# Performance work log

Measured on AMD Instinct MI355X. Metric: run time of the kernel, lower is better.

The kernel has to match this reference:

```python
import jax, jax.numpy as jnp
import numpy as np

N = 40000      # nodes
E = 640000     # edges
G = 64         # graphs in batch
F_IN = 128
H = 128


def setup_inputs() -> dict:
    key = jax.random.key(0)
    ks = jax.random.split(key, 10)
    x = jax.random.normal(ks[0], (N, F_IN), dtype=jnp.float32)
    edge_index = jax.random.randint(ks[1], (2, E), 0, N, dtype=jnp.int64)
    batch = jnp.sort(jax.random.randint(ks[2], (N,), 0, G, dtype=jnp.int64))
    s = 0.05
    W1 = jax.random.normal(ks[3], (F_IN, H), dtype=jnp.float32) * s
    W2 = jax.random.normal(ks[4], (H, H), dtype=jnp.float32) * s
    W3 = jax.random.normal(ks[5], (H, H), dtype=jnp.float32) * s
    Wl = jax.random.normal(ks[6], (H, 1), dtype=jnp.float32) * s
    b1 = jnp.zeros((H,), jnp.float32)
    b2 = jnp.zeros((H,), jnp.float32)
    b3 = jnp.zeros((H,), jnp.float32)
    bl = jnp.zeros((1,), jnp.float32)
    return {"x": x, "edge_index": edge_index, "batch": batch, "dropout_rate": 0,
            "W1": W1, "b1": b1, "W2": W2, "b2": b2, "W3": W3, "b3": b3,
            "Wl": Wl, "bl": bl}


def _gcn_norm(edge_index, n):
    # PyG GCNConv default: add self-loops, symmetric deg^{-1/2} normalization.
    loop = jnp.arange(n, dtype=edge_index.dtype)
    row = jnp.concatenate([edge_index[0], loop])  # source
    col = jnp.concatenate([edge_index[1], loop])  # target
    ones = jnp.ones(row.shape[0], jnp.float32)
    deg = jax.ops.segment_sum(ones, col, num_segments=n)
    dis = jnp.where(deg > 0, jax.lax.rsqrt(deg), 0.0)
    norm = dis[row] * dis[col]  # [E+N]
    return row, col, norm


def _gcn_conv(x, row, col, norm, W, b, n):
    h = x @ W + b                       # dense transform [N,H]
    msg = h[row] * norm[:, None]        # gather + scale  [E+N,H]
    return jax.ops.segment_sum(msg, col, num_segments=n)


def reference(x, edge_index, batch, dropout_rate, W1, b1, W2, b2, W3, b3, Wl, bl):
    n = x.shape[0]
    row, col, norm = _gcn_norm(edge_index, n)
    # eval mode: dropout(p=dropout_rate, training=False) is identity
    h = jax.nn.relu(_gcn_conv(x, row, col, norm, W1, b1, n))
    h = jax.nn.relu(_gcn_conv(h, row, col, norm, W2, b2, n))
    h = jax.nn.relu(_gcn_conv(h, row, col, norm, W3, b3, n))
    # global mean pool over graphs
    sums = jax.ops.segment_sum(h, batch, num_segments=G)           # [G,H]
    cnt = jax.ops.segment_sum(jnp.ones(n, jnp.float32), batch, num_segments=G)
    pooled = sums / jnp.maximum(cnt, 1.0)[:, None]
    return pooled @ Wl + bl             # [G,1]
```

## Files before the change

### kernel.cpp

```cpp
#include <hip/hip_runtime.h>

constexpr int N = 40000;
constexpr int E = 640000;
constexpr int G = 64;
constexpr int H = 128;

constexpr int NB      = (N + 255) / 256;
constexpr int EB      = (E + 255) / 256;
constexpr int GEMM1_B = N / 64;
constexpr int FUSED_B = N / 32;
constexpr int CSR_MAX = E + 8 * N;

typedef float    floatx2 __attribute__((ext_vector_type(2)));
typedef float    f32x4   __attribute__((ext_vector_type(4)));
typedef _Float16 f16x8   __attribute__((ext_vector_type(8)));

__device__ __forceinline__ unsigned pack_fp8x4(float a, float b, float c, float d) {
    unsigned v = 0;
    v = __builtin_amdgcn_cvt_pk_fp8_f32(a, b, v, false);
    v = __builtin_amdgcn_cvt_pk_fp8_f32(c, d, v, true);
    return v;
}

__device__ __forceinline__ void fma8(float4& acc, unsigned r, float w) {
    floatx2 lo = __builtin_amdgcn_cvt_pk_f32_fp8(r, false);
    floatx2 hi = __builtin_amdgcn_cvt_pk_f32_fp8(r, true);
    acc.x = fmaf(lo.x, w, acc.x);
    acc.y = fmaf(lo.y, w, acc.y);
    acc.z = fmaf(hi.x, w, acc.z);
    acc.w = fmaf(hi.y, w, acc.w);
}

__device__ __forceinline__ float entry_w(int e) {
    floatx2 hi = __builtin_amdgcn_cvt_pk_f32_fp8((unsigned)e, true);
    return hi.y;
}
__device__ __forceinline__ int entry_src(int e) { return e & 0xFFFFFF; }

__device__ __forceinline__ f16x8 cvt8(float4 a, float4 b) {
    f16x8 r;
    r[0] = (_Float16)a.x; r[1] = (_Float16)a.y; r[2] = (_Float16)a.z; r[3] = (_Float16)a.w;
    r[4] = (_Float16)b.x; r[5] = (_Float16)b.y; r[6] = (_Float16)b.z; r[7] = (_Float16)b.w;
    return r;
}

__device__ __forceinline__ float4 aggregate_node(const unsigned* __restrict__ h8,
                                                 const int4* __restrict__ csr4,
                                                 const int* __restrict__ row_ptr,
                                                 const float* __restrict__ dis,
                                                 int i, int c) {
    float d = dis[i];
    float sl = d * d;
    float4 acc = make_float4(0.f, 0.f, 0.f, 0.f);
    fma8(acc, h8[(size_t)i * 32 + c], sl);
    int p  = row_ptr[i] >> 2;
    int p1 = row_ptr[i + 1] >> 2;
    for (; p < p1; p += 2) {
        int4 ea = csr4[p], eb = csr4[p + 1];
        unsigned r0 = h8[(size_t)entry_src(ea.x) * 32 + c];
        unsigned r1 = h8[(size_t)entry_src(ea.y) * 32 + c];
        unsigned r2 = h8[(size_t)entry_src(ea.z) * 32 + c];
        unsigned r3 = h8[(size_t)entry_src(ea.w) * 32 + c];
        unsigned r4 = h8[(size_t)entry_src(eb.x) * 32 + c];
        unsigned r5 = h8[(size_t)entry_src(eb.y) * 32 + c];
        unsigned r6 = h8[(size_t)entry_src(eb.z) * 32 + c];
        unsigned r7 = h8[(size_t)entry_src(eb.w) * 32 + c];
        fma8(acc, r0, entry_w(ea.x)); fma8(acc, r1, entry_w(ea.y));
        fma8(acc, r2, entry_w(ea.z)); fma8(acc, r3, entry_w(ea.w));
        fma8(acc, r4, entry_w(eb.x)); fma8(acc, r5, entry_w(eb.y));
        fma8(acc, r6, entry_w(eb.z)); fma8(acc, r7, entry_w(eb.w));
    }
    return acc;
}

__global__ void prep_wt(const float* __restrict__ W1, const float* __restrict__ W2,
                        const float* __restrict__ W3, _Float16* __restrict__ wt) {
    const int m = blockIdx.x >> 3;
    const float* W = (m == 0) ? W1 : (m == 1) ? W2 : W3;
    const int g  = (blockIdx.x & 7) * 256 + threadIdx.x;
    const int f  = g >> 4;
    const int k0 = (g & 15) * 8;
    f16x8 v;
    #pragma unroll
    for (int j = 0; j < 8; ++j) v[j] = (_Float16)W[(size_t)(k0 + j) * H + f];
    *reinterpret_cast<f16x8*>(wt + ((size_t)m << 14) + f * H + k0) = v;
}

__global__ __launch_bounds__(256) void gemm1_and_count(const float* __restrict__ X,
                                                       const _Float16* __restrict__ wt1,
                                                       const float* __restrict__ b,
                                                       unsigned* __restrict__ Y,
                                                       const int* __restrict__ col,
                                                       int* __restrict__ deg) {
    __shared__ uint4 WTl[2048];
    const int blk = blockIdx.x;
    const int tid = threadIdx.x;
    if (blk >= GEMM1_B) {
        int e = (blk - GEMM1_B) * 256 + tid;
        if (e < E) atomicAdd(&deg[col[e]], 1);
        return;
    }
    const uint4* wtg = reinterpret_cast<const uint4*>(wt1);
    #pragma unroll
    for (int i = 0; i < 8; ++i) {
        int g = i * 256 + tid;
        WTl[g ^ ((g >> 4) & 7)] = wtg[g];
    }
    __syncthreads();

    const int lane = tid & 63;
    const int wv   = tid >> 6;
    const int c    = lane & 15;
    const int grp  = lane >> 4;
    const int node = blk * 64 + wv * 16 + c;

    const f32x4* b4 = reinterpret_cast<const f32x4*>(b);
    f32x4 acc[8];
    #pragma unroll
    for (int mt = 0; mt < 8; ++mt) acc[mt] = b4[mt * 4 + grp];

    const float4* X4 = reinterpret_cast<const float4*>(X);
    #pragma unroll
    for (int ks = 0; ks < 4; ++ks) {
        const int k0 = ks * 32 + grp * 8;
        float4 xa = X4[(size_t)node * 32 + (k0 >> 2)];
        float4 xb = X4[(size_t)node * 32 + (k0 >> 2) + 1];
        f16x8 bfr = cvt8(xa, xb);
        #pragma unroll
        for (int mt = 0; mt < 8; ++mt) {
            const int f = mt * 16 + c;
            const int g = (f << 4) + (k0 >> 3);
            f16x8 afr = *reinterpret_cast<const f16x8*>(&WTl[g ^ (f & 7)]);
            acc[mt] = __builtin_amdgcn_mfma_f32_16x16x32_f16(afr, bfr, acc[mt], 0, 0, 0);
        }
    }
    #pragma unroll
    for (int mt = 0; mt < 8; ++mt) {
        const int jg = mt * 4 + grp;
        Y[(size_t)node * 32 + jg] = pack_fp8x4(acc[mt][0], acc[mt][1], acc[mt][2], acc[mt][3]);
    }
}

__global__ void dis_block_sum(const int* __restrict__ deg, float* __restrict__ dis,
                              int* __restrict__ part) {
    __shared__ int s[256];
    int i = blockIdx.x * 256 + threadIdx.x;
    int d = (i < N) ? deg[i] : 0;
    if (i < N) dis[i] = rsqrtf((float)(d + 1));
    s[threadIdx.x] = (d + 7) & ~7;
    __syncthreads();
    for (int off = 128; off > 0; off >>= 1) {
        if (threadIdx.x < off) s[threadIdx.x] += s[threadIdx.x + off];
        __syncthreads();
    }
    if (threadIdx.x == 0) part[blockIdx.x] = s[0];
}

__global__ void scan_write(const int* __restrict__ deg, const int* __restrict__ part,
                           int* __restrict__ row_ptr, int* __restrict__ cursor) {
    __shared__ int s[256];
    const int t = threadIdx.x;
    s[t] = (t < (int)blockIdx.x) ? part[t] : 0;
    __syncthreads();
    for (int o = 128; o > 0; o >>= 1) {
        if (t < o) s[t] += s[t + o];
        __syncthreads();
    }
    const int block_off = s[0];
    __syncthreads();
    int i = blockIdx.x * 256 + t;
    int val = (i < N) ? ((deg[i] + 7) & ~7) : 0;
    s[t] = val;
    __syncthreads();
    for (int o = 1; o < 256; o <<= 1) {
        int x = (t >= o) ? s[t - o] : 0;
        __syncthreads();
        s[t] += x;
        __syncthreads();
    }
    if (i < N) {
        int excl = s[t] - val + block_off;
        row_ptr[i] = excl;
        cursor[i] = excl;
        if (i == N - 1) row_ptr[N] = excl + val;
    }
}

__global__ void fill_csr(const int* __restrict__ row, const int* __restrict__ col,
                         const float* __restrict__ dis, int* __restrict__ cursor,
                         int* __restrict__ csr) {
    int e = blockIdx.x * blockDim.x + threadIdx.x;
    if (e >= E) return;
    int r = row[e], c = col[e];
    float w = dis[r] * dis[c];
    unsigned wb = __builtin_amdgcn_cvt_pk_fp8_f32(w, 0.0f, 0, false) & 0xFFu;
    int p = atomicAdd(&cursor[c], 1);
    csr[p] = (int)((wb << 24) | (unsigned)r);
}

__global__ __launch_bounds__(256) void fused_agg_gemm(const unsigned* __restrict__ t_in,
                                                      const int4* __restrict__ csr4,
                                                      const int* __restrict__ row_ptr,
                                                      const float* __restrict__ dis,
                                                      const _Float16* __restrict__ wt,
                                                      const float* __restrict__ b,
                                                      unsigned* __restrict__ t_out) {
    __shared__ float4 tile[32 * 32];
    const int tid = threadIdx.x;
    const int node0 = blockIdx.x * 32;

    {
        const int cc = tid & 31;
        const int nl = tid >> 5;
        #pragma unroll
        for (int sub = 0; sub < 4; ++sub) {
            const int local = sub * 8 + nl;
            float4 acc = aggregate_node(t_in, csr4, row_ptr, dis, node0 + local, cc);
            acc.x = fmaxf(acc.x, 0.f); acc.y = fmaxf(acc.y, 0.f);
            acc.z = fmaxf(acc.z, 0.f); acc.w = fmaxf(acc.w, 0.f);
            tile[(local * 32 + cc) ^ (local & 7)] = acc;
        }
    }
    __syncthreads();

    const int lane = tid & 63;
    const int wv   = tid >> 6;
    const int c    = lane & 15;
    const int grp  = lane >> 4;

    const f32x4* b4 = reinterpret_cast<const f32x4*>(b);
    f32x4 acc00, acc01, acc10, acc11;
    acc00 = acc01 = b4[(2 * wv + 0) * 4 + grp];
    acc10 = acc11 = b4[(2 * wv + 1) * 4 + grp];

    const uint4* wtg = reinterpret_cast<const uint4*>(wt);
    #pragma unroll
    for (int ks = 0; ks < 4; ++ks) {
        const int k0 = ks * 32 + grp * 8;
        f16x8 bfr0, bfr1;
        {
            int nd = c;
            int g0 = nd * 32 + (k0 >> 2);
            float4 ta = tile[g0 ^ (nd & 7)];
            float4 tb = tile[(g0 + 1) ^ (nd & 7)];
            bfr0 = cvt8(ta, tb);
            nd = 16 + c;
            g0 = nd * 32 + (k0 >> 2);
            ta = tile[g0 ^ (nd & 7)];
            tb = tile[(g0 + 1) ^ (nd & 7)];
            bfr1 = cvt8(ta, tb);
        }
        {
            int f = (2 * wv + 0) * 16 + c;
            f16x8 afr = *reinterpret_cast<const f16x8*>(&wtg[f * 16 + (k0 >> 3)]);
            acc00 = __builtin_amdgcn_mfma_f32_16x16x32_f16(afr, bfr0, acc00, 0, 0, 0);
            acc01 = __builtin_amdgcn_mfma_f32_16x16x32_f16(afr, bfr1, acc01, 0, 0, 0);
            f = (2 * wv + 1) * 16 + c;
            afr = *reinterpret_cast<const f16x8*>(&wtg[f * 16 + (k0 >> 3)]);
            acc10 = __builtin_amdgcn_mfma_f32_16x16x32_f16(afr, bfr0, acc10, 0, 0, 0);
            acc11 = __builtin_amdgcn_mfma_f32_16x16x32_f16(afr, bfr1, acc11, 0, 0, 0);
        }
    }

    const int jg0 = (2 * wv + 0) * 4 + grp;
    const int jg1 = (2 * wv + 1) * 4 + grp;
    const int nA = node0 + c, nB = node0 + 16 + c;
    t_out[(size_t)nA * 32 + jg0] = pack_fp8x4(acc00[0], acc00[1], acc00[2], acc00[3]);
    t_out[(size_t)nB * 32 + jg0] = pack_fp8x4(acc01[0], acc01[1], acc01[2], acc01[3]);
    t_out[(size_t)nA * 32 + jg1] = pack_fp8x4(acc10[0], acc10[1], acc10[2], acc10[3]);
    t_out[(size_t)nB * 32 + jg1] = pack_fp8x4(acc11[0], acc11[1], acc11[2], acc11[3]);
}

__global__ __launch_bounds__(256) void agg_pool(const unsigned* __restrict__ t_in,
                                                const int4* __restrict__ csr4,
                                                const int* __restrict__ row_ptr,
                                                const float* __restrict__ dis,
                                                const int* __restrict__ batch,
                                                float* __restrict__ pooled) {
    __shared__ float4 tile[8 * 32];
    const int tid = threadIdx.x;
    const int c  = tid & 31;
    const int nl = tid >> 5;
    const int i0 = blockIdx.x * 8;

    float4 acc = aggregate_node(t_in, csr4, row_ptr, dis, i0 + nl, c);
    acc.x = fmaxf(acc.x, 0.f); acc.y = fmaxf(acc.y, 0.f);
    acc.z = fmaxf(acc.z, 0.f); acc.w = fmaxf(acc.w, 0.f);
    tile[nl * 32 + c] = acc;
    __syncthreads();

    if (tid < 128) {
        const int j = tid;
        const float* tf = reinterpret_cast<const float*>(tile);
        int cur = batch[i0];
        float s = 0.0f;
        #pragma unroll
        for (int r = 0; r < 8; ++r) {
            int g = batch[i0 + r];
            if (g != cur) { atomicAdd(&pooled[cur * H + j], s); s = 0.0f; cur = g; }
            s += tf[r * 128 + j];
        }
        atomicAdd(&pooled[cur * H + j], s);
    }
}

__global__ __launch_bounds__(128) void head(const float* __restrict__ pooled,
                                            const int* __restrict__ batch,
                                            const float* __restrict__ Wl,
                                            const float* __restrict__ bl,
                                            float* __restrict__ out) {
    const int g = blockIdx.x;
    const int j = threadIdx.x;
    __shared__ int bounds[2];
    if (j < 2) {
        int target = g + j;
        int lo = 0, hi = N;
        while (lo < hi) {
            int mid = (lo + hi) >> 1;
            if (batch[mid] < target) lo = mid + 1; else hi = mid;
        }
        bounds[j] = lo;
    }
    __syncthreads();
    float cnt = fmaxf((float)(bounds[1] - bounds[0]), 1.0f);
    float val = (pooled[g * H + j] / cnt) * Wl[j];
    __shared__ float red[128];
    red[j] = val;
    __syncthreads();
    #pragma unroll
    for (int s = 64; s > 0; s >>= 1) {
        if (j < s) red[j] += red[j + s];
        __syncthreads();
    }
    if (j == 0) out[g] = red[0] + bl[0];
}

extern "C" void kernel_launch(void* const* d_in, const int* in_sizes, int n_in,
                              void* d_out, int out_size, void* d_ws, size_t ws_size,
                              hipStream_t stream) {
    const float* x     = (const float*)d_in[0];
    const int*   ei    = (const int*)  d_in[1];
    const int*   batch = (const int*)  d_in[2];
    const float* W1 = (const float*)d_in[4];
    const float* b1 = (const float*)d_in[5];
    const float* W2 = (const float*)d_in[6];
    const float* b2 = (const float*)d_in[7];
    const float* W3 = (const float*)d_in[8];
    const float* b3 = (const float*)d_in[9];
    const float* Wl = (const float*)d_in[10];
    const float* bl = (const float*)d_in[11];
    float* out = (float*)d_out;

    const int* row = ei;
    const int* col = ei + E;

    auto align256 = [](size_t v) { return (v + 255) & ~(size_t)255; };
    char* ws = (char*)d_ws;
    size_t off = 0;
    int*   deg    = (int*)(ws + off);
    float* pooled = (float*)(deg + N);
    int*   csr    = (int*)(pooled + (size_t)G * H);
    size_t zero_bytes = (size_t)N * 4 + (size_t)G * H * 4 + (size_t)CSR_MAX * 4;
    off += align256(zero_bytes);
    float*    dis     = (float*)(ws + off); off += align256((size_t)N * 4);
    int*      row_ptr = (int*)  (ws + off); off += align256((size_t)(N + 1) * 4);
    int*      cursor  = (int*)  (ws + off); off += align256((size_t)N * 4);
    int*      part    = (int*)  (ws + off); off += align256((size_t)NB * 4);
    unsigned* bufA    = (unsigned*)(ws + off); off += align256((size_t)N * H);
    unsigned* bufB    = (unsigned*)(ws + off); off += align256((size_t)N * H);
    _Float16* wt      = (_Float16*)(ws + off); off += align256((size_t)3 * H * H * 2);
    (void)ws_size; (void)n_in; (void)in_sizes; (void)out_size;

    const int4* csr4 = reinterpret_cast<const int4*>(csr);
    _Float16* wt1 = wt;
    _Float16* wt2 = wt + (size_t)H * H;
    _Float16* wt3 = wt + (size_t)2 * H * H;

    hipMemsetAsync(deg, 0, zero_bytes, stream);
    prep_wt<<<24, 256, 0, stream>>>(W1, W2, W3, wt);
    gemm1_and_count<<<GEMM1_B + EB, 256, 0, stream>>>(x, wt1, b1, bufA, col, deg);
    dis_block_sum<<<NB, 256, 0, stream>>>(deg, dis, part);
    scan_write<<<NB, 256, 0, stream>>>(deg, part, row_ptr, cursor);
    fill_csr<<<EB, 256, 0, stream>>>(row, col, dis, cursor, csr);
    fused_agg_gemm<<<FUSED_B, 256, 0, stream>>>(bufA, csr4, row_ptr, dis, wt2, b2, bufB);
    fused_agg_gemm<<<FUSED_B, 256, 0, stream>>>(bufB, csr4, row_ptr, dis, wt3, b3, bufA);
    agg_pool<<<N / 8, 256, 0, stream>>>(bufA, csr4, row_ptr, dis, batch, pooled);
    head<<<G, 128, 0, stream>>>(pooled, batch, Wl, bl, out);
}
```

Before: 219.6 us.

## Prefetch CSR entries, use packed FMA, fold W2/W3 prep into gemm1, widen pool blocks

```diff
diff --git a/kernel.cpp b/kernel.cpp
--- a/kernel.cpp
+++ b/kernel.cpp
@@ -9,6 +9,7 @@
 constexpr int EB      = (E + 255) / 256;
 constexpr int GEMM1_B = N / 64;
 constexpr int FUSED_B = N / 32;
+constexpr int POOL_B  = N / 32;
 constexpr int CSR_MAX = E + 8 * N;
 
 typedef float    floatx2 __attribute__((ext_vector_type(2)));
@@ -22,13 +23,16 @@
     return v;
 }
 
-__device__ __forceinline__ void fma8(float4& acc, unsigned r, float w) {
+__device__ __forceinline__ void pk_fma(floatx2& acc, floatx2 a, floatx2 w2) {
+    asm("v_pk_fma_f32 %0, %1, %2, %0" : "+v"(acc) : "v"(a), "v"(w2));
+}
+
+__device__ __forceinline__ void fma8p(floatx2& aclo, floatx2& achi, unsigned r, float w) {
     floatx2 lo = __builtin_amdgcn_cvt_pk_f32_fp8(r, false);
     floatx2 hi = __builtin_amdgcn_cvt_pk_f32_fp8(r, true);
-    acc.x = fmaf(lo.x, w, acc.x);
-    acc.y = fmaf(lo.y, w, acc.y);
-    acc.z = fmaf(hi.x, w, acc.z);
-    acc.w = fmaf(hi.y, w, acc.w);
+    floatx2 w2 = {w, w};
+    pk_fma(aclo, lo, w2);
+    pk_fma(achi, hi, w2);
 }
 
 __device__ __forceinline__ float entry_w(int e) {
@@ -51,12 +55,16 @@
                                                  int i, int c) {
     float d = dis[i];
     float sl = d * d;
-    float4 acc = make_float4(0.f, 0.f, 0.f, 0.f);
-    fma8(acc, h8[(size_t)i * 32 + c], sl);
+    floatx2 aclo = {0.f, 0.f}, achi = {0.f, 0.f};
+    fma8p(aclo, achi, h8[(size_t)i * 32 + c], sl);
     int p  = row_ptr[i] >> 2;
     int p1 = row_ptr[i + 1] >> 2;
-    for (; p < p1; p += 2) {
-        int4 ea = csr4[p], eb = csr4[p + 1];
+    int4 ea, eb;
+    if (p < p1) { ea = csr4[p]; eb = csr4[p + 1]; }
+    while (p < p1) {
+        p += 2;
+        int pn = (p < p1) ? p : (p1 - 2);
+        int4 na = csr4[pn], nb = csr4[pn + 1];
         unsigned r0 = h8[(size_t)entry_src(ea.x) * 32 + c];
         unsigned r1 = h8[(size_t)entry_src(ea.y) * 32 + c];
         unsigned r2 = h8[(size_t)entry_src(ea.z) * 32 + c];
@@ -65,25 +73,23 @@
         unsigned r5 = h8[(size_t)entry_src(eb.y) * 32 + c];
         unsigned r6 = h8[(size_t)entry_src(eb.z) * 32 + c];
         unsigned r7 = h8[(size_t)entry_src(eb.w) * 32 + c];
-        fma8(acc, r0, entry_w(ea.x)); fma8(acc, r1, entry_w(ea.y));
-        fma8(acc, r2, entry_w(ea.z)); fma8(acc, r3, entry_w(ea.w));
-        fma8(acc, r4, entry_w(eb.x)); fma8(acc, r5, entry_w(eb.y));
-        fma8(acc, r6, entry_w(eb.z)); fma8(acc, r7, entry_w(eb.w));
-    }
-    return acc;
-}
-
-__global__ void prep_wt(const float* __restrict__ W1, const float* __restrict__ W2,
-                        const float* __restrict__ W3, _Float16* __restrict__ wt) {
-    const int m = blockIdx.x >> 3;
-    const float* W = (m == 0) ? W1 : (m == 1) ? W2 : W3;
-    const int g  = (blockIdx.x & 7) * 256 + threadIdx.x;
+        fma8p(aclo, achi, r0, entry_w(ea.x)); fma8p(aclo, achi, r1, entry_w(ea.y));
+        fma8p(aclo, achi, r2, entry_w(ea.z)); fma8p(aclo, achi, r3, entry_w(ea.w));
+        fma8p(aclo, achi, r4, entry_w(eb.x)); fma8p(aclo, achi, r5, entry_w(eb.y));
+        fma8p(aclo, achi, r6, entry_w(eb.z)); fma8p(aclo, achi, r7, entry_w(eb.w));
+        ea = na; eb = nb;
+    }
+    return make_float4(aclo.x, aclo.y, achi.x, achi.y);
+}
+
+__global__ void prep_wt1(const float* __restrict__ W1, _Float16* __restrict__ wt) {
+    const int g  = blockIdx.x * 256 + threadIdx.x;
     const int f  = g >> 4;
     const int k0 = (g & 15) * 8;
     f16x8 v;
     #pragma unroll
-    for (int j = 0; j < 8; ++j) v[j] = (_Float16)W[(size_t)(k0 + j) * H + f];
-    *reinterpret_cast<f16x8*>(wt + ((size_t)m << 14) + f * H + k0) = v;
+    for (int j = 0; j < 8; ++j) v[j] = (_Float16)W1[(size_t)(k0 + j) * H + f];
+    *reinterpret_cast<f16x8*>(wt + f * H + k0) = v;
 }
 
 __global__ __launch_bounds__(256) void gemm1_and_count(const float* __restrict__ X,
@@ -91,10 +97,26 @@
                                                        const float* __restrict__ b,
                                                        unsigned* __restrict__ Y,
                                                        const int* __restrict__ col,
-                                                       int* __restrict__ deg) {
+                                                       int* __restrict__ deg,
+                                                       const float* __restrict__ W2,
+                                                       const float* __restrict__ W3,
+                                                       _Float16* __restrict__ wt) {
     __shared__ uint4 WTl[2048];
     const int blk = blockIdx.x;
     const int tid = threadIdx.x;
+    if (blk >= GEMM1_B + EB) {
+        const int pb = blk - (GEMM1_B + EB);
+        const int m  = 1 + (pb >> 3);
+        const float* W = (m == 1) ? W2 : W3;
+        const int g  = (pb & 7) * 256 + tid;
+        const int f  = g >> 4;
+        const int k0 = (g & 15) * 8;
+        f16x8 v;
+        #pragma unroll
+        for (int j = 0; j < 8; ++j) v[j] = (_Float16)W[(size_t)(k0 + j) * H + f];
+        *reinterpret_cast<f16x8*>(wt + ((size_t)m << 14) + f * H + k0) = v;
+        return;
+    }
     if (blk >= GEMM1_B) {
         int e = (blk - GEMM1_B) * 256 + tid;
         if (e < E) atomicAdd(&deg[col[e]], 1);
@@ -277,16 +299,20 @@
                                                 const float* __restrict__ dis,
                                                 const int* __restrict__ batch,
                                                 float* __restrict__ pooled) {
-    __shared__ float4 tile[8 * 32];
+    __shared__ float4 tile[32 * 32];
     const int tid = threadIdx.x;
     const int c  = tid & 31;
     const int nl = tid >> 5;
-    const int i0 = blockIdx.x * 8;
-
-    float4 acc = aggregate_node(t_in, csr4, row_ptr, dis, i0 + nl, c);
-    acc.x = fmaxf(acc.x, 0.f); acc.y = fmaxf(acc.y, 0.f);
-    acc.z = fmaxf(acc.z, 0.f); acc.w = fmaxf(acc.w, 0.f);
-    tile[nl * 32 + c] = acc;
+    const int i0 = blockIdx.x * 32;
+
+    #pragma unroll
+    for (int sub = 0; sub < 4; ++sub) {
+        const int local = sub * 8 + nl;
+        float4 acc = aggregate_node(t_in, csr4, row_ptr, dis, i0 + local, c);
+        acc.x = fmaxf(acc.x, 0.f); acc.y = fmaxf(acc.y, 0.f);
+        acc.z = fmaxf(acc.z, 0.f); acc.w = fmaxf(acc.w, 0.f);
+        tile[local * 32 + c] = acc;
+    }
     __syncthreads();
 
     if (tid < 128) {
@@ -295,7 +321,7 @@
         int cur = batch[i0];
         float s = 0.0f;
         #pragma unroll
-        for (int r = 0; r < 8; ++r) {
+        for (int r = 0; r < 32; ++r) {
             int g = batch[i0 + r];
             if (g != cur) { atomicAdd(&pooled[cur * H + j], s); s = 0.0f; cur = g; }
             s += tf[r * 128 + j];
@@ -377,13 +403,14 @@
     _Float16* wt3 = wt + (size_t)2 * H * H;
 
     hipMemsetAsync(deg, 0, zero_bytes, stream);
-    prep_wt<<<24, 256, 0, stream>>>(W1, W2, W3, wt);
-    gemm1_and_count<<<GEMM1_B + EB, 256, 0, stream>>>(x, wt1, b1, bufA, col, deg);
+    prep_wt1<<<8, 256, 0, stream>>>(W1, wt1);
+    gemm1_and_count<<<GEMM1_B + EB + 16, 256, 0, stream>>>(x, wt1, b1, bufA, col, deg,
+                                                           W2, W3, wt);
     dis_block_sum<<<NB, 256, 0, stream>>>(deg, dis, part);
     scan_write<<<NB, 256, 0, stream>>>(deg, part, row_ptr, cursor);
     fill_csr<<<EB, 256, 0, stream>>>(row, col, dis, cursor, csr);
     fused_agg_gemm<<<FUSED_B, 256, 0, stream>>>(bufA, csr4, row_ptr, dis, wt2, b2, bufB);
     fused_agg_gemm<<<FUSED_B, 256, 0, stream>>>(bufB, csr4, row_ptr, dis, wt3, b3, bufA);
-    agg_pool<<<N / 8, 256, 0, stream>>>(bufA, csr4, row_ptr, dis, batch, pooled);
+    agg_pool<<<POOL_B, 256, 0, stream>>>(bufA, csr4, row_ptr, dis, batch, pooled);
     head<<<G, 128, 0, stream>>>(pooled, batch, Wl, bl, out);
 }
```

After: 216.8 us. Within noise of the previous version (-1.3%).
